# Performance work log

Measured on AMD Instinct MI355X. Metric: run time of the kernel, lower is better.

## Reference

```python
import jax, jax.numpy as jnp
import numpy as np

D = 4096          # in_features == out_features (scale broadcast requires square W)
TOKENS = 16384


def setup_inputs() -> dict:
    key = jax.random.key(0)
    kx, kq, ks, kb = jax.random.split(key, 4)
    x = jax.random.normal(kx, (TOKENS, D), dtype=jnp.float32)
    # int4 quantized weights in [-8, 7] (stored int8 in torch; int32 here is fine)
    qweight = jax.random.randint(kq, (D, D), -8, 8, dtype=jnp.int32)
    # per-channel scales: positive, realistic magnitude ~ max|W|/7
    scale = jax.random.uniform(ks, (D,), dtype=jnp.float32, minval=1e-3, maxval=2e-2)
    bias = jax.random.normal(kb, (D,), dtype=jnp.float32)
    return {"x": x, "qweight": qweight, "scale": scale, "bias": bias}


def reference(x, qweight, scale, bias):
    # Dequantize: W[i, j] = qW[i, j] * scale[i]  (scale.view(-1,1) in the source)
    W = qweight.astype(jnp.float32) * scale[:, None]   # [out, in]
    # F.linear(x, W, bias) = x @ W.T + bias
    return x @ W.T + bias                               # [tokens, out]
```

## Files before the change

### kernel.cpp

```cpp
#include <hip/hip_runtime.h>

typedef __attribute__((ext_vector_type(4))) int  i8x16;
typedef __attribute__((ext_vector_type(4))) int  i32x4;
typedef __attribute__((ext_vector_type(8))) short bf16x8;
typedef __attribute__((ext_vector_type(8))) unsigned short ushort8;
typedef __attribute__((ext_vector_type(4))) float f32x4;

__device__ __forceinline__ unsigned short f32_to_bf16(float f) {
    union { float f; unsigned int u; } v;
    v.f = f;
    unsigned int r = v.u + (0x7fffu + ((v.u >> 16) & 1u));
    return (unsigned short)(r >> 16);
}

__device__ __forceinline__ void gload_lds16(const void* g, void* l) {
    __builtin_amdgcn_global_load_lds(
        (const __attribute__((address_space(1))) unsigned int*)g,
        (__attribute__((address_space(3))) unsigned int*)l, 16, 0, 0);
}

__global__ __launch_bounds__(256) void quantx_kernel(const float* __restrict__ x,
                                                     char* __restrict__ xq,
                                                     float* __restrict__ rs, int K) {
    const int row = blockIdx.x;
    const float4* xr = (const float4*)(x + (size_t)row * K);
    const int K4 = K >> 2;
    const int t = threadIdx.x;
    float am = 0.f;
    for (int i = t; i < K4; i += 256) {
        float4 v = xr[i];
        am = fmaxf(am, fmaxf(fmaxf(fabsf(v.x), fabsf(v.y)),
                             fmaxf(fabsf(v.z), fabsf(v.w))));
    }
    for (int off = 32; off; off >>= 1) am = fmaxf(am, __shfl_xor(am, off));
    __shared__ float ws[4];
    if ((t & 63) == 0) ws[t >> 6] = am;
    __syncthreads();
    am = fmaxf(fmaxf(ws[0], ws[1]), fmaxf(ws[2], ws[3]));
    const float inv = am > 0.f ? 127.f / am : 0.f;
    if (t == 0) rs[row] = am > 0.f ? am / 127.f : 0.f;
    int* dst = (int*)(xq + (size_t)row * K);
    for (int i = t; i < K4; i += 256) {
        float4 v = xr[i];
        int a = (int)rintf(v.x * inv), b = (int)rintf(v.y * inv);
        int c = (int)rintf(v.z * inv), d = (int)rintf(v.w * inv);
        dst[i] = (a & 255) | ((b & 255) << 8) | ((c & 255) << 16) | (d << 24);
    }
}

__global__ void convq_kernel(const int* __restrict__ q, char* __restrict__ qb, long n16) {
    long i = (long)blockIdx.x * blockDim.x + threadIdx.x;
    const long stride = (long)gridDim.x * blockDim.x;
    for (; i < n16; i += stride) {
        const int4* p = (const int4*)(q + i * 16);
        int4 a = p[0], b = p[1], c = p[2], d = p[3];
        int4 r;
        r.x = (a.x & 255) | ((a.y & 255) << 8) | ((a.z & 255) << 16) | (a.w << 24);
        r.y = (b.x & 255) | ((b.y & 255) << 8) | ((b.z & 255) << 16) | (b.w << 24);
        r.z = (c.x & 255) | ((c.y & 255) << 8) | ((c.z & 255) << 16) | (c.w << 24);
        r.w = (d.x & 255) | ((d.y & 255) << 8) | ((d.z & 255) << 16) | (d.w << 24);
        ((int4*)qb)[i] = r;
    }
}

__global__ __launch_bounds__(512, 4) void qgemm_i8_kernel(
    const char* __restrict__ A, const char* __restrict__ B,
    const float* __restrict__ rs, const float* __restrict__ scale,
    const float* __restrict__ bias, float* __restrict__ C, int M, int N, int K) {
    extern __shared__ char sm[];

    const int tid  = threadIdx.x;
    const int lane = tid & 63;
    const int w    = tid >> 6;
    const int wr   = w >> 1;
    const int wc   = w & 1;
    const int l15  = lane & 15;
    const int l4   = lane >> 4;

    const int nwg = gridDim.x;
    const int bid = blockIdx.x;
    const int swz = (bid & 7) * (nwg >> 3) + (bid >> 3);
    const int nbn = N >> 7;
    const int m0  = (swz / nbn) << 8;
    const int n0  = (swz % nbn) << 7;

    const size_t srcO = (size_t)(tid >> 2) * K +
                        (size_t)(((tid & 3) ^ ((tid >> 3) & 3)) << 4);
    const int ldsO = w << 10;

    const char* pA = A + (size_t)m0 * K;
    const char* pB = B + (size_t)n0 * K;
    const size_t hK = (size_t)128 * K;
    const int NT = K >> 6;

#define STAGE(Ab, Bb, kt) do {                                   \
        gload_lds16(pA + srcO + (size_t)(kt) * 64, (Ab) + ldsO); \
        gload_lds16(pA + srcO + hK + (size_t)(kt) * 64, (Ab) + ldsO + 8192); \
        gload_lds16(pB + srcO + (size_t)(kt) * 64, (Bb) + ldsO); } while (0)

    const int slot  = (l4 ^ ((l15 >> 1) & 3)) << 4;
    const int aBase = (wr * 64 + l15) * 64 + slot;
    const int bBase = (wc * 64 + l15) * 64 + slot;

    i32x4 acc[4][4];
#pragma unroll
    for (int mf = 0; mf < 4; ++mf)
#pragma unroll
        for (int nf = 0; nf < 4; ++nf) acc[mf][nf] = (i32x4){0, 0, 0, 0};

    STAGE(sm + 0, sm + 32768, 0);
    if (NT > 1) {
        STAGE(sm + 16384, sm + 40960, 1);
        asm volatile("s_waitcnt vmcnt(3)" ::: "memory");
    } else {
        asm volatile("s_waitcnt vmcnt(0)" ::: "memory");
    }
    __builtin_amdgcn_s_barrier();

    for (int t = 0; t < NT; ++t) {
        char* Ab = sm + (t & 1) * 16384;
        char* Bb = sm + 32768 + (t & 1) * 8192;

        i8x16 aF[4], bF[4];
#pragma unroll
        for (int mf = 0; mf < 4; ++mf)
            aF[mf] = *(const i8x16*)(Ab + aBase + mf * 1024);
#pragma unroll
        for (int nf = 0; nf < 4; ++nf)
            bF[nf] = *(const i8x16*)(Bb + bBase + nf * 1024);
        asm volatile("s_waitcnt lgkmcnt(0)" ::: "memory");
        __builtin_amdgcn_sched_barrier(0);
        __builtin_amdgcn_s_setprio(1);
#pragma unroll
        for (int mf = 0; mf < 4; ++mf)
#pragma unroll
            for (int nf = 0; nf < 4; ++nf)
                acc[mf][nf] = __builtin_amdgcn_mfma_i32_16x16x64_i8(
                    aF[mf], bF[nf], acc[mf][nf], 0, 0, 0);
        __builtin_amdgcn_s_setprio(0);

        if (t + 1 < NT) {
            __builtin_amdgcn_s_barrier();
            if (t + 2 < NT) {
                STAGE(Ab, Bb, t + 2);
                asm volatile("s_waitcnt vmcnt(3)" ::: "memory");
            } else {
                asm volatile("s_waitcnt vmcnt(0)" ::: "memory");
            }
            __builtin_amdgcn_s_barrier();
        }
    }

#pragma unroll
    for (int mf = 0; mf < 4; ++mf) {
        const int row0 = m0 + wr * 64 + mf * 16 + l4 * 4;
        float rsv[4];
#pragma unroll
        for (int j = 0; j < 4; ++j) rsv[j] = rs[row0 + j];
#pragma unroll
        for (int nf = 0; nf < 4; ++nf) {
            const int col = n0 + wc * 64 + nf * 16 + l15;
            const float sc = scale[col];
            const float bs = bias[col];
#pragma unroll
            for (int j = 0; j < 4; ++j)
                C[(size_t)(row0 + j) * N + col] =
                    (float)acc[mf][nf][j] * (rsv[j] * sc) + bs;
        }
    }
#undef STAGE
}

__global__ __launch_bounds__(256) void qgemm_fb_kernel(
    const float* __restrict__ Af, const int* __restrict__ Bi,
    const float* __restrict__ scale, const float* __restrict__ bias,
    float* __restrict__ C, int M, int N, int K) {
    constexpr int BK = 64;
    __shared__ unsigned short lA[128 * BK];
    __shared__ unsigned short lB[128 * BK];
    const int t = threadIdx.x, lane = t & 63, w = t >> 6;
    const int wr = w >> 1, wc = w & 1;
    const int m0 = blockIdx.y * 128, n0 = blockIdx.x * 128;
    const int l15 = lane & 15, l4 = lane >> 4;
    f32x4 acc[4][4];
#pragma unroll
    for (int m = 0; m < 4; ++m)
#pragma unroll
        for (int n = 0; n < 4; ++n) acc[m][n] = (f32x4){0.f, 0.f, 0.f, 0.f};
    for (int k0 = 0; k0 < K; k0 += BK) {
        __syncthreads();
#pragma unroll
        for (int i = 0; i < 4; ++i) {
            const int off = i * 4096 + w * 1024 + lane * 16;
            const int row = off >> 7;
            const int col = (off & 127) >> 1;
            const float* pa = Af + (size_t)(m0 + row) * K + k0 + col;
            float4 a0 = *(const float4*)pa;
            float4 a1 = *(const float4*)(pa + 4);
            ushort8 va;
            va[0] = f32_to_bf16(a0.x); va[1] = f32_to_bf16(a0.y);
            va[2] = f32_to_bf16(a0.z); va[3] = f32_to_bf16(a0.w);
            va[4] = f32_to_bf16(a1.x); va[5] = f32_to_bf16(a1.y);
            va[6] = f32_to_bf16(a1.z); va[7] = f32_to_bf16(a1.w);
            *(ushort8*)((char*)lA + off) = va;
            const int* pb = Bi + (size_t)(n0 + row) * K + k0 + col;
            int4 b0 = *(const int4*)pb;
            int4 b1 = *(const int4*)(pb + 4);
            ushort8 vb;
            vb[0] = f32_to_bf16((float)b0.x); vb[1] = f32_to_bf16((float)b0.y);
            vb[2] = f32_to_bf16((float)b0.z); vb[3] = f32_to_bf16((float)b0.w);
            vb[4] = f32_to_bf16((float)b1.x); vb[5] = f32_to_bf16((float)b1.y);
            vb[6] = f32_to_bf16((float)b1.z); vb[7] = f32_to_bf16((float)b1.w);
            *(ushort8*)((char*)lB + off) = vb;
        }
        __syncthreads();
#pragma unroll
        for (int kk = 0; kk < BK; kk += 32) {
            bf16x8 af[4], bfr[4];
#pragma unroll
            for (int m = 0; m < 4; ++m)
                af[m] = *(const bf16x8*)&lA[(wr * 64 + m * 16 + l15) * BK + kk + l4 * 8];
#pragma unroll
            for (int n = 0; n < 4; ++n)
                bfr[n] = *(const bf16x8*)&lB[(wc * 64 + n * 16 + l15) * BK + kk + l4 * 8];
#pragma unroll
            for (int m = 0; m < 4; ++m)
#pragma unroll
                for (int n = 0; n < 4; ++n)
                    acc[m][n] = __builtin_amdgcn_mfma_f32_16x16x32_bf16(
                        af[m], bfr[n], acc[m][n], 0, 0, 0);
        }
    }
#pragma unroll
    for (int n = 0; n < 4; ++n) {
        const int col = n0 + wc * 64 + n * 16 + l15;
        const float sc = scale[col], bs = bias[col];
#pragma unroll
        for (int m = 0; m < 4; ++m) {
            const int row0 = m0 + wr * 64 + m * 16 + l4 * 4;
#pragma unroll
            for (int j = 0; j < 4; ++j)
                C[(size_t)(row0 + j) * N + col] = fmaf(acc[m][n][j], sc, bs);
        }
    }
}

extern "C" void kernel_launch(void* const* d_in, const int* in_sizes, int n_in,
                              void* d_out, int out_size, void* d_ws, size_t ws_size,
                              hipStream_t stream) {
    const float* x     = (const float*)d_in[0];
    const int*   q     = (const int*)d_in[1];
    const float* scale = (const float*)d_in[2];
    const float* bias  = (const float*)d_in[3];
    float*       out   = (float*)d_out;

    const int K = in_sizes[2];
    const int N = in_sizes[1] / K;
    const int M = in_sizes[0] / K;

    const size_t xq_b = (size_t)M * K;
    const size_t qb_b = (size_t)N * K;
    const size_t need = xq_b + qb_b + (size_t)M * 4;
    const int nwg = (M / 256) * (N / 128);

    if (ws_size >= need && (M % 256) == 0 && (N % 128) == 0 &&
        (K % 64) == 0 && K >= 128 && (nwg % 8) == 0) {
        char*  xq = (char*)d_ws;
        char*  qb = xq + xq_b;
        float* rs = (float*)(qb + qb_b);
        quantx_kernel<<<M, 256, 0, stream>>>(x, xq, rs, K);
        convq_kernel<<<2048, 256, 0, stream>>>(q, qb, (long)(qb_b / 16));
        qgemm_i8_kernel<<<nwg, 512, 49152, stream>>>(xq, qb, rs, scale, bias,
                                                     out, M, N, K);
    } else {
        dim3 grid(N / 128, M / 128);
        qgemm_fb_kernel<<<grid, 256, 0, stream>>>(x, q, scale, bias, out, M, N, K);
    }
}
```

Measured before the change: 404.5 us.

## Enlarge int8 GEMM tile to 256x256x128 with 4 waves and split LDS reads

Restructures the int8 MFMA GEMM from a 256x128 tile with 8 waves (64x64 per wave) to a 256x256 tile with 4 waves, each computing 128x128 with a 128-deep K step. Double-buffered LDS grows to 128 KB, and the fragment reads are split into two halves so the second half's LDS loads overlap the first half's MFMAs. The aim is more arithmetic per LDS and global byte and fewer barriers per unit of work. In exchange it holds 256 accumulator registers per lane and runs one block per CU, which lowers occupancy and raises register pressure and spill risk.

Result: slower. 513.9 us (+27.0%).

```diff
diff --git a/kernel.cpp b/kernel.cpp
--- a/kernel.cpp
+++ b/kernel.cpp
@@ -63,7 +63,7 @@
     }
 }
 
-__global__ __launch_bounds__(512, 4) void qgemm_i8_kernel(
+__global__ __launch_bounds__(256, 1) void qgemm_i8_kernel(
     const char* __restrict__ A, const char* __restrict__ B,
     const float* __restrict__ rs, const float* __restrict__ scale,
     const float* __restrict__ bias, float* __restrict__ C, int M, int N, int K) {
@@ -76,74 +76,86 @@
     const int wc   = w & 1;
     const int l15  = lane & 15;
     const int l4   = lane >> 4;
+    const int r7   = l15 & 7;
 
     const int nwg = gridDim.x;
     const int bid = blockIdx.x;
     const int swz = (bid & 7) * (nwg >> 3) + (bid >> 3);
-    const int nbn = N >> 7;
-    const int m0  = (swz / nbn) << 8;
-    const int n0  = (swz % nbn) << 7;
-
-    const size_t srcO = (size_t)(tid >> 2) * K +
-                        (size_t)(((tid & 3) ^ ((tid >> 3) & 3)) << 4);
-    const int ldsO = w << 10;
+    const int nbx = N >> 8;
+    const int m0  = (swz / nbx) << 8;
+    const int n0  = (swz % nbx) << 8;
+
+    const size_t inv0 = (size_t)(tid >> 3) * K +
+                        (size_t)(((tid & 7) ^ ((tid >> 3) & 7)) << 4);
+    const int ldsW = w << 10;
+
+#define STAGE_T(buf, gsrc) do {                                               \
+    _Pragma("unroll") for (int j = 0; j < 8; ++j)                             \
+        gload_lds16((gsrc) + inv0 + (size_t)(32 * j) * K,                     \
+                    (buf) + j * 4096 + ldsW); } while (0)
+
+    const int aRow0 = (wr * 128 + l15) * 128;
+    const int bRow0 = (wc * 128 + l15) * 128;
+    const int sl0   = ((0 + l4) ^ r7) << 4;
+    const int sl1   = ((4 + l4) ^ r7) << 4;
 
     const char* pA = A + (size_t)m0 * K;
     const char* pB = B + (size_t)n0 * K;
-    const size_t hK = (size_t)128 * K;
-    const int NT = K >> 6;
-
-#define STAGE(Ab, Bb, kt) do {                                   \
-        gload_lds16(pA + srcO + (size_t)(kt) * 64, (Ab) + ldsO); \
-        gload_lds16(pA + srcO + hK + (size_t)(kt) * 64, (Ab) + ldsO + 8192); \
-        gload_lds16(pB + srcO + (size_t)(kt) * 64, (Bb) + ldsO); } while (0)
-
-    const int slot  = (l4 ^ ((l15 >> 1) & 3)) << 4;
-    const int aBase = (wr * 64 + l15) * 64 + slot;
-    const int bBase = (wc * 64 + l15) * 64 + slot;
-
-    i32x4 acc[4][4];
-#pragma unroll
-    for (int mf = 0; mf < 4; ++mf)
-#pragma unroll
-        for (int nf = 0; nf < 4; ++nf) acc[mf][nf] = (i32x4){0, 0, 0, 0};
-
-    STAGE(sm + 0, sm + 32768, 0);
+    const int NT = K >> 7;
+
+    i32x4 acc[8][8];
+#pragma unroll
+    for (int m = 0; m < 8; ++m)
+#pragma unroll
+        for (int n = 0; n < 8; ++n) acc[m][n] = (i32x4){0, 0, 0, 0};
+
+#define RD8(DST, BUF, ROW0, SL)                                               \
+    _Pragma("unroll") for (int f = 0; f < 8; ++f)                             \
+        (DST)[f] = *(const i8x16*)((BUF) + (ROW0) + f * 2048 + (SL));
+#define MFMA64(AF, BF)                                                        \
+    _Pragma("unroll") for (int m = 0; m < 8; ++m)                             \
+    _Pragma("unroll") for (int n = 0; n < 8; ++n)                             \
+        acc[m][n] = __builtin_amdgcn_mfma_i32_16x16x64_i8(                    \
+            (AF)[m], (BF)[n], acc[m][n], 0, 0, 0);
+#define LGKM(NM) do { asm volatile("s_waitcnt lgkmcnt(" #NM ")" ::: "memory");\
+                      __builtin_amdgcn_sched_barrier(0); } while (0)
+
+    i8x16 aF0[8], aF1[8], bF0[8], bF1[8];
+
+    STAGE_T(sm + 0,     pA);
+    STAGE_T(sm + 65536, pB);
     if (NT > 1) {
-        STAGE(sm + 16384, sm + 40960, 1);
-        asm volatile("s_waitcnt vmcnt(3)" ::: "memory");
+        STAGE_T(sm + 32768, pA + 128);
+        STAGE_T(sm + 98304, pB + 128);
+        asm volatile("s_waitcnt vmcnt(16)" ::: "memory");
     } else {
         asm volatile("s_waitcnt vmcnt(0)" ::: "memory");
     }
     __builtin_amdgcn_s_barrier();
 
     for (int t = 0; t < NT; ++t) {
-        char* Ab = sm + (t & 1) * 16384;
-        char* Bb = sm + 32768 + (t & 1) * 8192;
-
-        i8x16 aF[4], bF[4];
-#pragma unroll
-        for (int mf = 0; mf < 4; ++mf)
-            aF[mf] = *(const i8x16*)(Ab + aBase + mf * 1024);
-#pragma unroll
-        for (int nf = 0; nf < 4; ++nf)
-            bF[nf] = *(const i8x16*)(Bb + bBase + nf * 1024);
-        asm volatile("s_waitcnt lgkmcnt(0)" ::: "memory");
-        __builtin_amdgcn_sched_barrier(0);
+        char* Ab = sm + (t & 1) * 32768;
+        char* Bb = sm + 65536 + (t & 1) * 32768;
+
+        RD8(aF0, Ab, aRow0, sl0);
+        RD8(bF0, Bb, bRow0, sl0);
+        RD8(aF1, Ab, aRow0, sl1);
+        RD8(bF1, Bb, bRow0, sl1);
+        LGKM(15);
         __builtin_amdgcn_s_setprio(1);
-#pragma unroll
-        for (int mf = 0; mf < 4; ++mf)
-#pragma unroll
-            for (int nf = 0; nf < 4; ++nf)
-                acc[mf][nf] = __builtin_amdgcn_mfma_i32_16x16x64_i8(
-                    aF[mf], bF[nf], acc[mf][nf], 0, 0, 0);
+        MFMA64(aF0, bF0);
+        __builtin_amdgcn_s_setprio(0);
+        LGKM(0);
+        __builtin_amdgcn_s_setprio(1);
+        MFMA64(aF1, bF1);
         __builtin_amdgcn_s_setprio(0);
 
         if (t + 1 < NT) {
             __builtin_amdgcn_s_barrier();
             if (t + 2 < NT) {
-                STAGE(Ab, Bb, t + 2);
-                asm volatile("s_waitcnt vmcnt(3)" ::: "memory");
+                STAGE_T(Ab, pA + (size_t)(t + 2) * 128);
+                STAGE_T(Bb, pB + (size_t)(t + 2) * 128);
+                asm volatile("s_waitcnt vmcnt(16)" ::: "memory");
             } else {
                 asm volatile("s_waitcnt vmcnt(0)" ::: "memory");
             }
@@ -152,23 +164,23 @@
     }
 
 #pragma unroll
-    for (int mf = 0; mf < 4; ++mf) {
-        const int row0 = m0 + wr * 64 + mf * 16 + l4 * 4;
-        float rsv[4];
-#pragma unroll
-        for (int j = 0; j < 4; ++j) rsv[j] = rs[row0 + j];
-#pragma unroll
-        for (int nf = 0; nf < 4; ++nf) {
-            const int col = n0 + wc * 64 + nf * 16 + l15;
-            const float sc = scale[col];
-            const float bs = bias[col];
+    for (int n = 0; n < 8; ++n) {
+        const int col = n0 + wc * 128 + n * 16 + l15;
+        const float sc = scale[col];
+        const float bs = bias[col];
+#pragma unroll
+        for (int m = 0; m < 8; ++m) {
+            const int row0 = m0 + wr * 128 + m * 16 + l4 * 4;
 #pragma unroll
             for (int j = 0; j < 4; ++j)
                 C[(size_t)(row0 + j) * N + col] =
-                    (float)acc[mf][nf][j] * (rsv[j] * sc) + bs;
-        }
-    }
-#undef STAGE
+                    (float)acc[m][n][j] * (rs[row0 + j] * sc) + bs;
+        }
+    }
+#undef STAGE_T
+#undef RD8
+#undef MFMA64
+#undef LGKM
 }
 
 __global__ __launch_bounds__(256) void qgemm_fb_kernel(
@@ -261,17 +273,17 @@
     const size_t xq_b = (size_t)M * K;
     const size_t qb_b = (size_t)N * K;
     const size_t need = xq_b + qb_b + (size_t)M * 4;
-    const int nwg = (M / 256) * (N / 128);
-
-    if (ws_size >= need && (M % 256) == 0 && (N % 128) == 0 &&
-        (K % 64) == 0 && K >= 128 && (nwg % 8) == 0) {
+    const int nwg = (M / 256) * (N / 256);
+
+    if (ws_size >= need && (M % 256) == 0 && (N % 256) == 0 &&
+        (K % 128) == 0 && K >= 256 && (nwg % 8) == 0) {
         char*  xq = (char*)d_ws;
         char*  qb = xq + xq_b;
         float* rs = (float*)(qb + qb_b);
         quantx_kernel<<<M, 256, 0, stream>>>(x, xq, rs, K);
         convq_kernel<<<2048, 256, 0, stream>>>(q, qb, (long)(qb_b / 16));
-        qgemm_i8_kernel<<<nwg, 512, 49152, stream>>>(xq, qb, rs, scale, bias,
-                                                     out, M, N, K);
+        qgemm_i8_kernel<<<nwg, 256, 131072, stream>>>(xq, qb, rs, scale, bias,
+                                                      out, M, N, K);
     } else {
         dim3 grid(N / 128, M / 128);
         qgemm_fb_kernel<<<grid, 256, 0, stream>>>(x, q, scale, bias, out, M, N, K);
```
